# Kernel optimization log

Measured on AMD Instinct MI355X. Metric: run time of the kernel, lower is better.

Reference implementation:

```python
import jax, jax.numpy as jnp
import numpy as np

# Irreps config: input/output = 32x0e + 16x1o (dim 80), H=4 heads -> head = 8x0e + 4x1o (dim 20)
M0, M1 = 32, 16      # input muls for 0e / 1o
m0, m1 = 8, 4        # per-head muls
H = 4
HEAD_DIM = m0 + 3 * m1   # 20
WNUM = H * (M0 * m0 + M1 * m0 + M0 * m1 + M1 * m1)  # 2304 per-edge TP weights
NB, HID = 16, 64
SQRT3 = np.float32(np.sqrt(3.0))
EPS = 1e-8


def radial_mlp(x, W1, b1, W2, b2):
    return jax.nn.silu(x @ W1 + b1) @ W2 + b2


def tp_edge(ss, vv, sh0, sh1, w):
    """FullyConnectedTensorProduct (32x0e+16x1o) x (1x0e+1x1o) -> H*(8x0e+4x1o) with per-edge weights w [E, WNUM].
    Paths: 0e*0e->0e, 1o*1o->0e (CG dot/sqrt3), 0e*1o->1o, 1o*0e->1o; path norm 1/sqrt(fan_in)."""
    E = ss.shape[0]
    per = M0 * m0 + M1 * m0 + M0 * m1 + M1 * m1  # 576
    w = w.reshape(E, H, per)
    o = 0
    Wss = w[..., o:o + M0 * m0].reshape(E, H, M0, m0); o += M0 * m0
    Wvv = w[..., o:o + M1 * m0].reshape(E, H, M1, m0); o += M1 * m0
    Wsv = w[..., o:o + M0 * m1].reshape(E, H, M0, m1); o += M0 * m1
    Wvs = w[..., o:o + M1 * m1].reshape(E, H, M1, m1)
    fan = np.float32(np.sqrt(M0 + M1))  # fan_in = 48 for both output irreps
    vv_dot = jnp.einsum('eui,ei->eu', vv, sh1) / SQRT3
    out0 = (jnp.einsum('eu,ehuw->ehw', ss * sh0[:, None], Wss)
            + jnp.einsum('eu,ehuw->ehw', vv_dot, Wvv)) / fan          # [E,H,m0]
    out1 = (jnp.einsum('eu,ehuw->ehw', ss, Wsv)[..., None] * sh1[:, None, None, :]
            + jnp.einsum('eui,ehuw->ehwi', vv * sh0[:, None, None], Wvs)) / fan  # [E,H,m1,3]
    return out0, out1


def setup_inputs() -> dict:
    key = jax.random.key(0)
    ks = jax.random.split(key, 24)
    N, E = 2000, 32000
    g = lambda k, s, sc=1.0: jax.random.normal(k, s, jnp.float32) * sc
    inp = {}
    inp['node_features'] = g(ks[0], (N, M0 + 3 * M1))
    inp['edge_index'] = jax.random.randint(ks[1], (2, E), 0, N)
    inp['edge_sh'] = g(ks[2], (E, 4))
    inp['edge_radial_emb'] = jax.random.uniform(ks[3], (E, NB), jnp.float32)
    # query e3nn Linear (per-head blocks)
    inp['Wq0'] = g(ks[4], (H, M0, m0))
    inp['Wq1'] = g(ks[5], (H, M1, m1))
    # radial MLPs for key / value TP weights
    inp['Wk1'] = g(ks[6], (NB, HID), 1 / np.sqrt(NB)); inp['bk1'] = jnp.zeros((HID,), jnp.float32)
    inp['Wk2'] = g(ks[7], (HID, WNUM), 1 / np.sqrt(HID)); inp['bk2'] = jnp.zeros((WNUM,), jnp.float32)
    inp['Wv1'] = g(ks[8], (NB, HID), 1 / np.sqrt(NB)); inp['bv1'] = jnp.zeros((HID,), jnp.float32)
    inp['Wv2'] = g(ks[9], (HID, WNUM), 1 / np.sqrt(HID)); inp['bv2'] = jnp.zeros((WNUM,), jnp.float32)
    # single-head dot-product TP -> 0e (shared weights)
    inp['Wd0'] = g(ks[10], (m0, m0))
    inp['Wd1'] = g(ks[11], (m1, m1))
    # output projection Linear (all heads mixed per irrep)
    inp['Wo0'] = g(ks[12], (H * m0, M0))
    inp['Wo1'] = g(ks[13], (H * m1, M1))
    # FFN: out irreps -> (2*M0)x0e + M1x1o -> out irreps
    inp['Wf1_0'] = g(ks[14], (M0, 2 * M0))
    inp['Wf1_1'] = g(ks[15], (M1, M1))
    inp['Wf2_0'] = g(ks[16], (2 * M0, M0))
    inp['Wf2_1'] = g(ks[17], (M1, M1))
    return inp


def reference(node_features, edge_index, edge_sh, edge_radial_emb,
              Wq0, Wq1, Wk1, bk1, Wk2, bk2, Wv1, bv1, Wv2, bv2,
              Wd0, Wd1, Wo0, Wo1, Wf1_0, Wf1_1, Wf2_0, Wf2_1):
    N = node_features.shape[0]
    s = node_features[:, :M0]                       # [N, M0] scalars
    v = node_features[:, M0:].reshape(N, M1, 3)     # [N, M1, 3] vectors
    src, dst = edge_index[0], edge_index[1]

    # query Linear (e3nn: per-irrep channel mix, norm 1/sqrt(fan_in))
    q0 = jnp.einsum('nu,huw->nhw', s, Wq0) / np.sqrt(M0)
    q1 = jnp.einsum('nui,huw->nhwi', v, Wq1) / np.sqrt(M1)

    sh0, sh1 = edge_sh[:, 0], edge_sh[:, 1:4]
    ss, vv = s[src], v[src]                         # gather per edge

    wk = radial_mlp(edge_radial_emb, Wk1, bk1, Wk2, bk2)
    wv = radial_mlp(edge_radial_emb, Wv1, bv1, Wv2, bv2)
    k0, k1 = tp_edge(ss, vv, sh0, sh1, wk)
    v0, v1 = tp_edge(ss, vv, sh0, sh1, wv)

    # per-head equivariant dot product -> 0e logits
    qd0, qd1 = q0[dst], q1[dst]
    fan_d = np.float32(np.sqrt(m0 * m0 + m1 * m1))
    logits = (jnp.einsum('ehu,uv,ehv->eh', qd0, Wd0, k0)
              + jnp.einsum('ehui,uv,ehvi->eh', qd1, Wd1, k1) / SQRT3) / fan_d
    logits = logits / np.sqrt(HEAD_DIM)             # self.scale
    logits = jnp.clip(logits, -10.0, 10.0)

    # scatter softmax over edges sharing a destination node
    seg_max = jax.ops.segment_max(logits, dst, num_segments=N)
    seg_max = jnp.maximum(seg_max, -10.0)           # handle empty segments
    ex = jnp.exp(logits - seg_max[dst])
    denom = jax.ops.segment_sum(ex, dst, num_segments=N)
    alpha = ex / (denom[dst] + 1e-12)               # [E, H]

    agg0 = jax.ops.segment_sum(alpha[..., None] * v0, dst, num_segments=N)        # [N,H,m0]
    agg1 = jax.ops.segment_sum(alpha[..., None, None] * v1, dst, num_segments=N)  # [N,H,m1,3]

    # output projection Linear over concatenated heads
    o0 = agg0.reshape(N, H * m0) @ Wo0 / np.sqrt(H * m0)
    o1 = jnp.einsum('nui,uw->nwi', agg1.reshape(N, H * m1, 3), Wo1) / np.sqrt(H * m1)

    # residual (input irreps == output irreps -> identity skip)
    x0 = s + o0
    x1 = v + o1

    # FFN with SafeNormActivation
    f0 = x0 @ Wf1_0 / np.sqrt(M0)                               # [N, 2*M0]
    f1 = jnp.einsum('nui,uw->nwi', x1, Wf1_1) / np.sqrt(M1)     # [N, M1, 3]
    a0 = jax.nn.silu(f0)
    norms = jnp.linalg.norm(f1, axis=-1, keepdims=True)
    safe = jnp.maximum(norms, EPS)
    a1 = jnp.where(norms < EPS, 0.0, (f1 / safe) * jax.nn.silu(norms))
    g0 = a0 @ Wf2_0 / np.sqrt(2 * M0)
    g1 = jnp.einsum('nui,uw->nwi', a1, Wf2_1) / np.sqrt(M1)

    out0 = x0 + g0
    out1 = x1 + g1
    return jnp.concatenate([out0, out1.reshape(N, M1 * 3)], axis=-1)
```

## Files before the change

kernel.cpp:

```cpp
#include <hip/hip_runtime.h>

typedef unsigned int uint;
typedef unsigned short ushort;
typedef __attribute__((ext_vector_type(8))) short bf16x8;
typedef __attribute__((ext_vector_type(4))) float f32x4;
typedef __attribute__((ext_vector_type(2))) float f32x2;

#define N_NODES 2000
#define N_EDGES 32000
#define WNUM 2304

constexpr size_t OFF_AGG0 = 0;
constexpr size_t OFF_AGG1 = 64000;
constexpr size_t OFF_DEN  = 160000;
constexpr size_t OFF_FLAG = 170000;
constexpr size_t OFF_W2T  = 170004;
constexpr size_t OFF_QT0  = 317460;
constexpr size_t OFF_QT1  = 381460;
constexpr size_t OFF_W1T  = 509460;
constexpr size_t OFF_W1P  = 511508;

__device__ __forceinline__ float b2f(ushort u){ union{uint i; float f;}x; x.i=((uint)u)<<16; return x.f; }
__device__ __forceinline__ float lo16(uint w){ union{uint u; float f;}x; x.u=w<<16; return x.f; }
__device__ __forceinline__ float hi16(uint w){ union{uint u; float f;}x; x.u=w&0xFFFF0000u; return x.f; }
__device__ __forceinline__ ushort f2b(float f){
  union{float f; uint u;}x; x.f=f;
  uint r = (x.u + 0x7FFFu + ((x.u>>16)&1u)) >> 16;
  return (ushort)r;
}
__device__ __forceinline__ float siluf(float x){ return x / (1.f + __expf(-x)); }

template<bool F32>
__device__ __forceinline__ float ldf(const void* p, int i){
  if (F32) return ((const float*)p)[i];
  return b2f(((const ushort*)p)[i]);
}
__device__ __forceinline__ float ldfr(const void* p, int i, bool f32){
  return f32 ? ((const float*)p)[i] : b2f(((const ushort*)p)[i]);
}

template<bool F32>
__device__ void prep_body(
    const void* __restrict__ nf,
    const void* __restrict__ Wk2, const void* __restrict__ Wv2,
    const void* __restrict__ Wk1, const void* __restrict__ Wv1,
    const void* __restrict__ Wq0, const void* __restrict__ Wq1,
    const void* __restrict__ Wd0, const void* __restrict__ Wd1,
    ushort* __restrict__ W2T, float* __restrict__ W1T, uint* __restrict__ W1P,
    float* __restrict__ qt0, float* __restrict__ qt1){
  const int t = threadIdx.x;
  const int bid = blockIdx.x;

  if (bid < 72){
    __shared__ ushort tile[64][66];
    const int mat = bid / 36, jt = bid - mat*36;
    const void* W = mat ? Wv2 : Wk2;
    const int j0 = jt*64;
    const int jo = t & 63, cb = t >> 6;
    #pragma unroll
    for (int k=0; k<16; ++k){
      const int c = cb + k*4;
      tile[c][jo] = F32 ? f2b(((const float*)W)[(size_t)c*WNUM + j0 + jo])
                        : ((const ushort*)W)[(size_t)c*WNUM + j0 + jo];
    }
    __syncthreads();
    const int jl = t >> 2, c0 = (t & 3)*16;
    ushort* dst = W2T + (size_t)mat*147456 + (size_t)(j0+jl)*64 + c0;
    #pragma unroll
    for (int k=0; k<16; ++k) dst[k] = tile[c0+k][jl];
  } else if (bid < 104){
    __shared__ float nfL[64][80];
    __shared__ float wq0L[1024], wq1L[256], wd0L[64], wd1L[16];
    const int nb = bid - 72, n0 = nb*64;
    for (int idx=t; idx<64*80; idx+=256){
      const int nn = n0 + idx/80;
      nfL[idx/80][idx%80] = (nn < N_NODES) ? ldf<F32>(nf, nn*80 + idx%80) : 0.f;
    }
    for (int idx=t; idx<1024; idx+=256) wq0L[idx] = ldf<F32>(Wq0, idx);
    if (t < 256) wq1L[t] = ldf<F32>(Wq1, t);
    if (t < 64)  wd0L[t] = ldf<F32>(Wd0, t);
    if (t < 16)  wd1L[t] = ldf<F32>(Wd1, t);
    __syncthreads();
    const int nl = t >> 2, h = t & 3;
    const int nn = n0 + nl;
    if (nn < N_NODES){
      const float* S = &nfL[nl][0];
      float q0[8];
      #pragma unroll
      for (int w=0; w<8; ++w){
        float a = 0.f;
        #pragma unroll
        for (int u=0; u<32; ++u) a += S[u]*wq0L[h*256 + u*8 + w];
        q0[w] = a * 0.17677669529663687f;
      }
      #pragma unroll
      for (int vv=0; vv<8; ++vv){
        float a = 0.f;
        #pragma unroll
        for (int u=0; u<8; ++u) a += q0[u]*wd0L[u*8+vv];
        qt0[nn*32 + h*8 + vv] = a;
      }
      float q1[12];
      #pragma unroll
      for (int w=0; w<4; ++w)
        #pragma unroll
        for (int i=0; i<3; ++i){
          float a = 0.f;
          #pragma unroll
          for (int u=0; u<16; ++u) a += S[32+u*3+i]*wq1L[h*64 + u*4 + w];
          q1[w*3+i] = a * 0.25f;
        }
      #pragma unroll
      for (int vv=0; vv<4; ++vv)
        #pragma unroll
        for (int i=0; i<3; ++i){
          float a = 0.f;
          #pragma unroll
          for (int u=0; u<4; ++u) a += q1[u*3+i]*wd1L[u*4+vv];
          qt1[nn*48 + h*12 + vv*3 + i] = a;
        }
    }
  } else {
    for (int idx=t; idx<2048; idx+=256){
      const int mat = idx >> 10, rem = idx & 1023;
      const int c = rem >> 4, b = rem & 15;
      W1T[idx] = ldf<F32>(mat ? Wv1 : Wk1, b*64 + c);
    }
    for (int idx=t; idx<1024; idx+=256){
      const int mat = idx >> 9, rem = idx & 511;
      const int c = rem >> 3, j = rem & 7;
      const void* W = mat ? Wv1 : Wk1;
      ushort u0, u1;
      if (F32){ u0 = f2b(((const float*)W)[(2*j)*64+c]); u1 = f2b(((const float*)W)[(2*j+1)*64+c]); }
      else    { u0 = ((const ushort*)W)[(2*j)*64+c];     u1 = ((const ushort*)W)[(2*j+1)*64+c]; }
      W1P[idx] = (uint)u0 | ((uint)u1 << 16);
    }
  }
}

__global__ __launch_bounds__(256) void prep_kernel(
    const void* nf,
    const void* Wk2, const void* Wv2,
    const void* Wk1, const void* Wv1,
    const void* Wq0, const void* Wq1,
    const void* Wd0, const void* Wd1,
    ushort* W2T, float* W1T, uint* W1P, float* qt0, float* qt1,
    int* flag){
  __shared__ int s_cnt;
  const int t = threadIdx.x;
  if (t == 0) s_cnt = 0;
  __syncthreads();
  {
    uint u = ((const ushort*)nf)[t*2];
    uint ex = (u >> 7) & 0xFFu;
    if (ex >= 0xA0u) atomicAdd(&s_cnt, 1);
  }
  __syncthreads();
  const bool F32 = (s_cnt >= 20);
  if (blockIdx.x == 0 && t == 0) *flag = F32 ? 1 : 0;
  if (F32) prep_body<true >(nf, Wk2, Wv2, Wk1, Wv1, Wq0, Wq1, Wd0, Wd1, W2T, W1T, W1P, qt0, qt1);
  else     prep_body<false>(nf, Wk2, Wv2, Wk1, Wv1, Wq0, Wq1, Wd0, Wd1, W2T, W1T, W1P, qt0, qt1);
}

struct Smem {
  ushort hidA[4096];
  union {
    struct {
      float fssT[32][34];
      float fvvT[16][34];
      float sslT[32][34];
    } f;
    float cont[2688];
  } u;
  float vshT[3][16][34];
  float sh1T[3][34];
  int   dstL[32];
};

__device__ __forceinline__ f32x4 mma_pair(const bf16x8& a0f, const bf16x8& a1f,
                                          bf16x8 b0, bf16x8 b1, float bb){
  f32x4 c = {bb,bb,bb,bb};
  c = __builtin_amdgcn_mfma_f32_16x16x32_bf16(a0f, b0, c, 0,0,0);
  c = __builtin_amdgcn_mfma_f32_16x16x32_bf16(a1f, b1, c, 0,0,0);
  return c;
}
__device__ __forceinline__ void acc_feat(const f32x4 c, const float* fp, float* acc){
  f32x2 fA = *(const f32x2*)(fp);
  f32x2 fB = *(const f32x2*)(fp + 2);
  acc[0] += c[0]*fA[0]; acc[1] += c[1]*fA[1];
  acc[2] += c[2]*fB[0]; acc[3] += c[3]*fB[1];
}

template<bool F32>
__device__ void edge_body(
    const void* __restrict__ nf,  const int* __restrict__ eidx,
    const void* __restrict__ esh, const void* __restrict__ emb,
    const float* __restrict__ W1T, const uint* __restrict__ W1P,
    const void* __restrict__ bk1, const void* __restrict__ bk2,
    const void* __restrict__ bv1, const void* __restrict__ bv2,
    const ushort* __restrict__ W2T,
    const float* __restrict__ qt0g, const float* __restrict__ qt1g,
    float* __restrict__ agg0, float* __restrict__ agg1, float* __restrict__ denom,
    Smem& sm){
  const int t  = threadIdx.x;
  const int hw = t >> 5;
  const int r  = t & 31;
  const int geb = blockIdx.x*32;

  int geA[4], srcA[4], dstA[4];
  float shv0[4], shv1[4], shv2[4], shv3[4];
  #pragma unroll
  for (int e=0; e<4; ++e) geA[e] = geb + hw*4 + e;
  #pragma unroll
  for (int e=0; e<4; ++e){ srcA[e] = eidx[geA[e]]; dstA[e] = eidx[N_EDGES + geA[e]]; }
  #pragma unroll
  for (int e=0; e<4; ++e){
    if (F32){
      float4 s4 = ((const float4*)esh)[geA[e]];
      shv0[e]=s4.x; shv1[e]=s4.y; shv2[e]=s4.z; shv3[e]=s4.w;
    } else {
      uint2 u2 = ((const uint2*)esh)[geA[e]];
      shv0[e]=lo16(u2.x); shv1[e]=hi16(u2.x); shv2[e]=lo16(u2.y); shv3[e]=hi16(u2.y);
    }
  }
  #pragma unroll
  for (int e=0; e<4; ++e){
    const int le = hw*4+e, src = srcA[e];
    const float sh0 = shv0[e], s1a = shv1[e], s1b = shv2[e], s1c = shv3[e];
    if (r == 0) sm.dstL[le] = dstA[e];
    if (r < 3) sm.sh1T[r][le] = (r==0)? s1a : (r==1)? s1b : s1c;
    float sv = ldf<F32>(nf, src*80 + r);
    sm.u.f.sslT[r][le] = sv;
    sm.u.f.fssT[r][le] = sv * sh0;
    if (r < 16){
      float v0 = ldf<F32>(nf, src*80+32+r*3+0);
      float v1 = ldf<F32>(nf, src*80+32+r*3+1);
      float v2 = ldf<F32>(nf, src*80+32+r*3+2);
      sm.vshT[0][r][le] = v0*sh0; sm.vshT[1][r][le] = v1*sh0; sm.vshT[2][r][le] = v2*sh0;
      sm.u.f.fvvT[r][le] = (v0*s1a + v1*s1b + v2*s1c) * 0.5773502691896258f;
    }
  }

  {
    float bkv[2], bvv[2];
    f32x4 wkF[2][4], wvF[2][4];
    uint4 wkB[2][2], wvB[2][2];
    #pragma unroll
    for (int cc=0; cc<2; ++cc){
      const int c = r + cc*32;
      bkv[cc] = ldf<F32>(bk1, c); bvv[cc] = ldf<F32>(bv1, c);
      if (F32){
        const f32x4* pk = (const f32x4*)(W1T + c*16);
        const f32x4* pv = (const f32x4*)(W1T + 1024 + c*16);
        wkF[cc][0]=pk[0]; wkF[cc][1]=pk[1]; wkF[cc][2]=pk[2]; wkF[cc][3]=pk[3];
        wvF[cc][0]=pv[0]; wvF[cc][1]=pv[1]; wvF[cc][2]=pv[2]; wvF[cc][3]=pv[3];
      } else {
        const uint4* pk = (const uint4*)(W1P + c*8);
        const uint4* pv = (const uint4*)(W1P + 512 + c*8);
        wkB[cc][0]=pk[0]; wkB[cc][1]=pk[1];
        wvB[cc][0]=pv[0]; wvB[cc][1]=pv[1];
      }
    }
    uint4 ra, rb; float4 fa, fb, fc, fd;
    if (F32){
      const float4* p = (const float4*)emb + (size_t)geA[0]*4;
      fa = p[0]; fb = p[1]; fc = p[2]; fd = p[3];
    } else {
      const uint4* p = (const uint4*)emb + (size_t)geA[0]*2;
      ra = p[0]; rb = p[1];
    }
    #pragma unroll
    for (int e=0; e<4; ++e){
      float em[16];
      if (F32){
        em[0]=fa.x; em[1]=fa.y; em[2]=fa.z; em[3]=fa.w;
        em[4]=fb.x; em[5]=fb.y; em[6]=fb.z; em[7]=fb.w;
        em[8]=fc.x; em[9]=fc.y; em[10]=fc.z; em[11]=fc.w;
        em[12]=fd.x; em[13]=fd.y; em[14]=fd.z; em[15]=fd.w;
      } else {
        em[0]=lo16(ra.x); em[1]=hi16(ra.x); em[2]=lo16(ra.y); em[3]=hi16(ra.y);
        em[4]=lo16(ra.z); em[5]=hi16(ra.z); em[6]=lo16(ra.w); em[7]=hi16(ra.w);
        em[8]=lo16(rb.x); em[9]=hi16(rb.x); em[10]=lo16(rb.y); em[11]=hi16(rb.y);
        em[12]=lo16(rb.z); em[13]=hi16(rb.z); em[14]=lo16(rb.w); em[15]=hi16(rb.w);
      }
      if (e < 3){
        if (F32){
          const float4* p = (const float4*)emb + (size_t)geA[e+1]*4;
          fa = p[0]; fb = p[1]; fc = p[2]; fd = p[3];
        } else {
          const uint4* p = (const uint4*)emb + (size_t)geA[e+1]*2;
          ra = p[0]; rb = p[1];
        }
      }
      const int le = hw*4+e;
      #pragma unroll
      for (int cc=0; cc<2; ++cc){
        const int c = r + cc*32;
        float ak = bkv[cc], av = bvv[cc];
        if (F32){
          #pragma unroll
          for (int g=0; g<4; ++g)
            #pragma unroll
            for (int j=0; j<4; ++j){
              ak += em[g*4+j]*wkF[cc][g][j];
              av += em[g*4+j]*wvF[cc][g][j];
            }
        } else {
          #pragma unroll
          for (int g=0; g<2; ++g){
            const uint4 a = wkB[cc][g], b = wvB[cc][g];
            ak += em[g*8+0]*lo16(a.x) + em[g*8+1]*hi16(a.x)
                + em[g*8+2]*lo16(a.y) + em[g*8+3]*hi16(a.y)
                + em[g*8+4]*lo16(a.z) + em[g*8+5]*hi16(a.z)
                + em[g*8+6]*lo16(a.w) + em[g*8+7]*hi16(a.w);
            av += em[g*8+0]*lo16(b.x) + em[g*8+1]*hi16(b.x)
                + em[g*8+2]*lo16(b.y) + em[g*8+3]*hi16(b.y)
                + em[g*8+4]*lo16(b.z) + em[g*8+5]*hi16(b.z)
                + em[g*8+6]*lo16(b.w) + em[g*8+7]*hi16(b.w);
          }
        }
        const int idx = (le>>4)*1024 + (c>>5)*512 + ((((c>>3)&3)*16 + (le&15))<<3) + (c&7);
        sm.hidA[idx]        = f2b(siluf(ak));
        sm.hidA[2048 + idx] = f2b(siluf(av));
      }
    }
  }
  __syncthreads();

  const int h = t >> 6;
  const int lane = t & 63, q = lane >> 4, n = lane & 15;
  const float invfan = 0.14433756729740643f;
  float exv[2][4];

  const ushort* wbase = W2T + h*36864 + n*64 + q*8;
  const int bi0 = h*576 + n;
  const float* fb_ss = &sm.u.f.fssT[n>>3][q*4];
  const float* fb_sl = &sm.u.f.sslT[n>>2][q*4];
  const int nq2 = n>>2;

  #pragma unroll 1
  for (int kv=0; kv<2; ++kv){
    const ushort* wptr = wbase + kv*147456;
    const void* bvec = kv ? bv2 : bk2;
    bf16x8 af[2][2];
    #pragma unroll
    for (int Mt=0; Mt<2; ++Mt)
      #pragma unroll
      for (int kh=0; kh<2; ++kh)
        af[Mt][kh] = *(const bf16x8*)&sm.hidA[kv*2048 + Mt*1024 + kh*512 + lane*8];

    float a0[2][4], aP[2][4], aW[3][2][4];
    #pragma unroll
    for (int Mt=0; Mt<2; ++Mt)
      #pragma unroll
      for (int z=0; z<4; ++z){
        a0[Mt][z]=0.f; aP[Mt][z]=0.f;
        aW[0][Mt][z]=0.f; aW[1][Mt][z]=0.f; aW[2][Mt][z]=0.f;
      }

#define PREF(P0,P1,PB,TL) \
  P0 = *(const bf16x8*)(wptr + (TL)*1024); \
  P1 = *(const bf16x8*)(wptr + (TL)*1024 + 32); \
  PB = ldf<F32>(bvec, bi0 + (TL)*16);

    bf16x8 pA0, pA1, pB0, pB1; float pAb, pBb;
    PREF(pA0, pA1, pAb, 0);
    PREF(pB0, pB1, pBb, 1);

    #pragma unroll 2
    for (int tl=0; tl<24; tl+=2){
      { bf16x8 b0=pA0, b1=pA1; float bb=pAb;
        PREF(pA0, pA1, pAb, tl+2);
        const float* fp = fb_ss + tl*68;
        #pragma unroll
        for (int Mt=0; Mt<2; ++Mt) acc_feat(mma_pair(af[Mt][0], af[Mt][1], b0, b1, bb), fp + Mt*16, a0[Mt]); }
      { bf16x8 b0=pB0, b1=pB1; float bb=pBb;
        PREF(pB0, pB1, pBb, tl+3);
        const float* fp = fb_ss + (tl+1)*68;
        #pragma unroll
        for (int Mt=0; Mt<2; ++Mt) acc_feat(mma_pair(af[Mt][0], af[Mt][1], b0, b1, bb), fp + Mt*16, a0[Mt]); }
    }
    #pragma unroll 2
    for (int tl=24; tl<32; tl+=2){
      { bf16x8 b0=pA0, b1=pA1; float bb=pAb;
        PREF(pA0, pA1, pAb, tl+2);
        const float* fp = fb_sl + (tl-24)*136;
        #pragma unroll
        for (int Mt=0; Mt<2; ++Mt) acc_feat(mma_pair(af[Mt][0], af[Mt][1], b0, b1, bb), fp + Mt*16, aP[Mt]); }
      { bf16x8 b0=pB0, b1=pB1; float bb=pBb;
        PREF(pB0, pB1, pBb, tl+3);
        const float* fp = fb_sl + (tl-23)*136;
        #pragma unroll
        for (int Mt=0; Mt<2; ++Mt) acc_feat(mma_pair(af[Mt][0], af[Mt][1], b0, b1, bb), fp + Mt*16, aP[Mt]); }
    }
#define BODY_AW(B0,B1,BB,TL) { \
    const int u = ((TL)-32)*4 + nq2; \
    _Pragma("unroll") \
    for (int Mt=0; Mt<2; ++Mt){ \
      f32x4 c = mma_pair(af[Mt][0], af[Mt][1], B0, B1, BB); \
      _Pragma("unroll") \
      for (int i=0; i<3; ++i) acc_feat(c, &sm.vshT[i][u][Mt*16+q*4], aW[i][Mt]); \
    } }
    { bf16x8 b0=pA0, b1=pA1; float bb=pAb; PREF(pA0, pA1, pAb, 34); BODY_AW(b0,b1,bb,32); }
    { bf16x8 b0=pB0, b1=pB1; float bb=pBb; PREF(pB0, pB1, pBb, 35); BODY_AW(b0,b1,bb,33); }
    { bf16x8 b0=pA0, b1=pA1; float bb=pAb; BODY_AW(b0,b1,bb,34); }
    { bf16x8 b0=pB0, b1=pB1; float bb=pBb; BODY_AW(b0,b1,bb,35); }
#undef BODY_AW
#undef PREF

    #pragma unroll
    for (int Mt=0; Mt<2; ++Mt)
      #pragma unroll
      for (int z=0; z<4; ++z){
        a0[Mt][z] += __shfl_xor(a0[Mt][z], 8, 64);
        aP[Mt][z] += __shfl_xor(aP[Mt][z], 4, 64);
        aP[Mt][z] += __shfl_xor(aP[Mt][z], 8, 64);
        #pragma unroll
        for (int i=0; i<3; ++i){
          aW[i][Mt][z] += __shfl_xor(aW[i][Mt][z], 4, 64);
          aW[i][Mt][z] += __shfl_xor(aW[i][Mt][z], 8, 64);
        }
      }

    if (kv == 0){
      float lgp[2][4];
      #pragma unroll
      for (int Mt=0; Mt<2; ++Mt)
        #pragma unroll
        for (int z=0; z<4; ++z){
          const int el = Mt*16 + q*4 + z;
          const int d = sm.dstL[el];
          float acc = 0.f;
          if (n < 8) acc = qt0g[d*32 + h*8 + n] * a0[Mt][z];
          if (n < 4){
            float s = 0.f;
            #pragma unroll
            for (int i=0; i<3; ++i){
              float k1 = aP[Mt][z]*sm.sh1T[i][el] + aW[i][Mt][z];
              s += qt1g[d*48 + h*12 + n*3 + i] * k1;
            }
            acc += s * 0.5773502691896258f;
          }
          lgp[Mt][z] = acc;
        }
      #pragma unroll
      for (int Mt=0; Mt<2; ++Mt)
        #pragma unroll
        for (int z=0; z<4; ++z){
          lgp[Mt][z] += __shfl_xor(lgp[Mt][z], 1, 64);
          lgp[Mt][z] += __shfl_xor(lgp[Mt][z], 2, 64);
          lgp[Mt][z] += __shfl_xor(lgp[Mt][z], 4, 64);
          lgp[Mt][z] += __shfl_xor(lgp[Mt][z], 8, 64);
          float lg = lgp[Mt][z] * invfan * 0.025f;
          lg = fminf(10.f, fmaxf(-10.f, lg));
          exv[Mt][z] = __expf(lg - 10.0f);
        }
    } else {
      __syncthreads();
      #pragma unroll
      for (int Mt=0; Mt<2; ++Mt)
        #pragma unroll
        for (int z=0; z<4; ++z){
          const int el = Mt*16 + q*4 + z;
          const float ex = exv[Mt][z];
          float* cp = &sm.u.cont[el*84 + h*21];
          if (n == 0) cp[0] = ex;
          if (n < 8)  cp[1+n] = ex * a0[Mt][z] * invfan;
          if (n < 4){
            #pragma unroll
            for (int i=0; i<3; ++i){
              float v1 = (aP[Mt][z]*sm.sh1T[i][el] + aW[i][Mt][z]) * invfan;
              cp[9+n*3+i] = ex * v1;
            }
          }
        }
    }
  }
  __syncthreads();

  #pragma unroll
  for (int k=0; k<11; ++k){
    const int idx = t + k*256;
    if (idx < 2688){
      const int el = idx / 84;
      const int cm = idx - el*84;
      const int h2 = cm / 21;
      const int comp = cm - h2*21;
      const float val = sm.u.cont[idx];
      const int d2 = sm.dstL[el];
      if (comp == 0)      atomicAdd(denom + d2*4  + h2, val);
      else if (comp < 9)  atomicAdd(agg0  + d2*32 + h2*8  + (comp-1), val);
      else                atomicAdd(agg1  + d2*48 + h2*12 + (comp-9), val);
    }
  }
}

__global__ __launch_bounds__(256) void edge_kernel(
    const void* nf, const int* eidx, const void* esh, const void* emb,
    const float* W1T, const uint* W1P,
    const void* bk1, const void* bk2,
    const void* bv1, const void* bv2,
    const ushort* W2T, const float* qt0g, const float* qt1g,
    float* agg0, float* agg1, float* denom, const int* flag){
  __shared__ Smem sm;
  if (*flag)
    edge_body<true >(nf,eidx,esh,emb,W1T,W1P,bk1,bk2,bv1,bv2,W2T,qt0g,qt1g,agg0,agg1,denom,sm);
  else
    edge_body<false>(nf,eidx,esh,emb,W1T,W1P,bk1,bk2,bv1,bv2,W2T,qt0g,qt1g,agg0,agg1,denom,sm);
}

__global__ __launch_bounds__(256) void node_out_kernel(
    const void* __restrict__ nf, const float* __restrict__ agg0r, const float* __restrict__ agg1r,
    const float* __restrict__ denom,
    const void* __restrict__ Wo0, const void* __restrict__ Wo1,
    const void* __restrict__ Wf10, const void* __restrict__ Wf11,
    const void* __restrict__ Wf20, const void* __restrict__ Wf21,
    void* __restrict__ out, const int* __restrict__ flag){
  __shared__ float ag0[4][32], ag1[4][48], adiv[4][4];
  __shared__ float x0s[4][32], x1s[4][48], a0s[4][64], f1s[4][48], coefs[4][16];
  const bool F32 = (*flag) != 0;
  const int s = threadIdx.x >> 6, t = threadIdx.x & 63;
  const int n = blockIdx.x*4 + s;
  if (t < 4) adiv[s][t] = 1.f / (denom[n*4+t] + 1e-12f);
  __syncthreads();
  if (t < 32) ag0[s][t] = agg0r[n*32+t] * adiv[s][t>>3];
  if (t < 48) ag1[s][t] = agg1r[n*48+t] * adiv[s][t/12];
  __syncthreads();
  if (t < 32){
    float o = 0.f;
    #pragma unroll
    for (int k=0; k<32; ++k) o += ag0[s][k]*ldfr(Wo0, k*32+t, F32);
    x0s[s][t] = ldfr(nf, n*80+t, F32) + o*0.17677669529663687f;
  }
  if (t < 48){
    int w = t/3, i = t - w*3;
    float o = 0.f;
    #pragma unroll
    for (int u=0; u<16; ++u) o += ag1[s][u*3+i]*ldfr(Wo1, u*16+w, F32);
    x1s[s][t] = ldfr(nf, n*80+32+t, F32) + o*0.25f;
  }
  __syncthreads();
  {
    float f0 = 0.f;
    #pragma unroll
    for (int u=0; u<32; ++u) f0 += x0s[s][u]*ldfr(Wf10, u*64+t, F32);
    a0s[s][t] = siluf(f0*0.17677669529663687f);
  }
  if (t < 48){
    int w = t/3, i = t - w*3;
    float f1 = 0.f;
    #pragma unroll
    for (int u=0; u<16; ++u) f1 += x1s[s][u*3+i]*ldfr(Wf11, u*16+w, F32);
    f1s[s][t] = f1*0.25f;
  }
  __syncthreads();
  if (t < 16){
    float a = f1s[s][t*3], b = f1s[s][t*3+1], c = f1s[s][t*3+2];
    float nrm = sqrtf(a*a+b*b+c*c);
    float safe = fmaxf(nrm, 1e-8f);
    coefs[s][t] = (nrm < 1e-8f) ? 0.f : siluf(nrm)/safe;
  }
  __syncthreads();
  if (t < 32){
    float g = 0.f;
    #pragma unroll
    for (int u=0; u<64; ++u) g += a0s[s][u]*ldfr(Wf20, u*32+t, F32);
    float val = x0s[s][t] + g*0.125f;
    if (F32) ((float*)out)[n*80+t] = val; else ((ushort*)out)[n*80+t] = f2b(val);
  }
  if (t < 48){
    int w = t/3, i = t - w*3;
    float g = 0.f;
    #pragma unroll
    for (int u=0; u<16; ++u) g += coefs[s][u]*f1s[s][u*3+i]*ldfr(Wf21, u*16+w, F32);
    float val = x1s[s][t] + g*0.25f;
    if (F32) ((float*)out)[n*80+32+t] = val; else ((ushort*)out)[n*80+32+t] = f2b(val);
  }
}

extern "C" void kernel_launch(void* const* d_in, const int* in_sizes, int n_in,
                              void* d_out, int out_size, void* d_ws, size_t ws_size,
                              hipStream_t stream){
  const void* nf   = d_in[0];
  const int*  eidx = (const int*)d_in[1];
  const void* esh  = d_in[2];
  const void* emb  = d_in[3];
  const void* Wq0  = d_in[4];
  const void* Wq1  = d_in[5];
  const void* Wk1  = d_in[6];
  const void* bk1  = d_in[7];
  const void* Wk2  = d_in[8];
  const void* bk2  = d_in[9];
  const void* Wv1  = d_in[10];
  const void* bv1  = d_in[11];
  const void* Wv2  = d_in[12];
  const void* bv2  = d_in[13];
  const void* Wd0  = d_in[14];
  const void* Wd1  = d_in[15];
  const void* Wo0  = d_in[16];
  const void* Wo1  = d_in[17];
  const void* Wf10 = d_in[18];
  const void* Wf11 = d_in[19];
  const void* Wf20 = d_in[20];
  const void* Wf21 = d_in[21];
  float* ws = (float*)d_ws;

  float* agg0  = ws + OFF_AGG0;
  float* agg1  = ws + OFF_AGG1;
  float* denom = ws + OFF_DEN;
  int*   flag  = (int*)(ws + OFF_FLAG);
  ushort* W2T  = (ushort*)(ws + OFF_W2T);
  float* qt0   = ws + OFF_QT0;
  float* qt1   = ws + OFF_QT1;
  float* W1T   = ws + OFF_W1T;
  uint*  W1P   = (uint*)(ws + OFF_W1P);

  hipMemsetAsync(agg0, 0, 168000*sizeof(float), stream);
  prep_kernel<<<105, 256, 0, stream>>>(nf, Wk2, Wv2, Wk1, Wv1, Wq0, Wq1, Wd0, Wd1,
                                       W2T, W1T, W1P, qt0, qt1, flag);
  edge_kernel<<<N_EDGES/32, 256, 0, stream>>>(nf, eidx, esh, emb,
                                              W1T, W1P, bk1, bk2, bv1, bv2,
                                              W2T, qt0, qt1,
                                              agg0, agg1, denom, flag);
  node_out_kernel<<<N_NODES/4, 256, 0, stream>>>(nf, agg0, agg1, denom,
                                                 Wo0, Wo1, Wf10, Wf11, Wf20, Wf21, d_out, flag);
}
```

Measured before the change: 219.9 us.

## Process 64 edges per block with key/value waves running concurrently

The edge kernel now handles 64 edges per 512-thread block instead of 32 per 256 threads. Each wave owns one (key/value, head) pair, so the key and value MFMA passes run in parallel on separate waves rather than in a serial loop. Per-edge intermediates are parked in shared memory and the softmax exponentials pass through an LDS buffer. Each W2 B-fragment load now feeds four M-tiles instead of two, halving global weight traffic per edge, at the cost of more LDS, more registers and fewer blocks in flight.

```diff
diff --git a/kernel.cpp b/kernel.cpp
--- a/kernel.cpp
+++ b/kernel.cpp
@@ -163,18 +163,21 @@
 }
 
 struct Smem {
-  ushort hidA[4096];
+  ushort hidA[8192];
   union {
     struct {
-      float fssT[32][34];
-      float fvvT[16][34];
-      float sslT[32][34];
+      float fssT[32][66];
+      float fvvT[16][66];
+      float sslT[32][66];
     } f;
-    float cont[2688];
+    float cont[5376];
   } u;
-  float vshT[3][16][34];
-  float sh1T[3][34];
-  int   dstL[32];
+  float vshT[3][16][66];
+  float sh1T[3][66];
+  float park0[2][4][64][8];
+  float parkP[2][4][64][4];
+  float exL[64][4];
+  int   dstL[64];
 };
 
 __device__ __forceinline__ f32x4 mma_pair(const bf16x8& a0f, const bf16x8& a1f,
@@ -203,74 +206,73 @@
     float* __restrict__ agg0, float* __restrict__ agg1, float* __restrict__ denom,
     Smem& sm){
   const int t  = threadIdx.x;
-  const int hw = t >> 5;
-  const int r  = t & 31;
-  const int geb = blockIdx.x*32;
-
-  int geA[4], srcA[4], dstA[4];
-  float shv0[4], shv1[4], shv2[4], shv3[4];
-  #pragma unroll
-  for (int e=0; e<4; ++e) geA[e] = geb + hw*4 + e;
-  #pragma unroll
-  for (int e=0; e<4; ++e){ srcA[e] = eidx[geA[e]]; dstA[e] = eidx[N_EDGES + geA[e]]; }
-  #pragma unroll
-  for (int e=0; e<4; ++e){
+  const int geb = blockIdx.x*64;
+
+  {
+    const int g = t >> 5, r = t & 31;
+    int geA[4], srcA[4], dstA[4];
+    float shv0[4], shv1[4], shv2[4], shv3[4];
+    #pragma unroll
+    for (int e=0; e<4; ++e) geA[e] = geb + g*4 + e;
+    #pragma unroll
+    for (int e=0; e<4; ++e){ srcA[e] = eidx[geA[e]]; dstA[e] = eidx[N_EDGES + geA[e]]; }
+    #pragma unroll
+    for (int e=0; e<4; ++e){
+      if (F32){
+        float4 s4 = ((const float4*)esh)[geA[e]];
+        shv0[e]=s4.x; shv1[e]=s4.y; shv2[e]=s4.z; shv3[e]=s4.w;
+      } else {
+        uint2 u2 = ((const uint2*)esh)[geA[e]];
+        shv0[e]=lo16(u2.x); shv1[e]=hi16(u2.x); shv2[e]=lo16(u2.y); shv3[e]=hi16(u2.y);
+      }
+    }
+    #pragma unroll
+    for (int e=0; e<4; ++e){
+      const int le = g*4+e, src = srcA[e];
+      const float sh0 = shv0[e], s1a = shv1[e], s1b = shv2[e], s1c = shv3[e];
+      if (r == 0) sm.dstL[le] = dstA[e];
+      if (r < 3) sm.sh1T[r][le] = (r==0)? s1a : (r==1)? s1b : s1c;
+      float sv = ldf<F32>(nf, src*80 + r);
+      sm.u.f.sslT[r][le] = sv;
+      sm.u.f.fssT[r][le] = sv * sh0;
+      if (r < 16){
+        float v0 = ldf<F32>(nf, src*80+32+r*3+0);
+        float v1 = ldf<F32>(nf, src*80+32+r*3+1);
+        float v2 = ldf<F32>(nf, src*80+32+r*3+2);
+        sm.vshT[0][r][le] = v0*sh0; sm.vshT[1][r][le] = v1*sh0; sm.vshT[2][r][le] = v2*sh0;
+        sm.u.f.fvvT[r][le] = (v0*s1a + v1*s1b + v2*s1c) * 0.5773502691896258f;
+      }
+    }
+  }
+
+  {
+    const int c  = t & 63;
+    const int g8 = t >> 6;
+    const int le0 = g8*8;
+    float bkv = ldf<F32>(bk1, c), bvv = ldf<F32>(bv1, c);
+    f32x4 wkF[4], wvF[4];
+    uint4 wkB[2], wvB[2];
     if (F32){
-      float4 s4 = ((const float4*)esh)[geA[e]];
-      shv0[e]=s4.x; shv1[e]=s4.y; shv2[e]=s4.z; shv3[e]=s4.w;
+      const f32x4* pk = (const f32x4*)(W1T + c*16);
+      const f32x4* pv = (const f32x4*)(W1T + 1024 + c*16);
+      wkF[0]=pk[0]; wkF[1]=pk[1]; wkF[2]=pk[2]; wkF[3]=pk[3];
+      wvF[0]=pv[0]; wvF[1]=pv[1]; wvF[2]=pv[2]; wvF[3]=pv[3];
     } else {
-      uint2 u2 = ((const uint2*)esh)[geA[e]];
-      shv0[e]=lo16(u2.x); shv1[e]=hi16(u2.x); shv2[e]=lo16(u2.y); shv3[e]=hi16(u2.y);
-    }
-  }
-  #pragma unroll
-  for (int e=0; e<4; ++e){
-    const int le = hw*4+e, src = srcA[e];
-    const float sh0 = shv0[e], s1a = shv1[e], s1b = shv2[e], s1c = shv3[e];
-    if (r == 0) sm.dstL[le] = dstA[e];
-    if (r < 3) sm.sh1T[r][le] = (r==0)? s1a : (r==1)? s1b : s1c;
-    float sv = ldf<F32>(nf, src*80 + r);
-    sm.u.f.sslT[r][le] = sv;
-    sm.u.f.fssT[r][le] = sv * sh0;
-    if (r < 16){
-      float v0 = ldf<F32>(nf, src*80+32+r*3+0);
-      float v1 = ldf<F32>(nf, src*80+32+r*3+1);
-      float v2 = ldf<F32>(nf, src*80+32+r*3+2);
-      sm.vshT[0][r][le] = v0*sh0; sm.vshT[1][r][le] = v1*sh0; sm.vshT[2][r][le] = v2*sh0;
-      sm.u.f.fvvT[r][le] = (v0*s1a + v1*s1b + v2*s1c) * 0.5773502691896258f;
-    }
-  }
-
-  {
-    float bkv[2], bvv[2];
-    f32x4 wkF[2][4], wvF[2][4];
-    uint4 wkB[2][2], wvB[2][2];
-    #pragma unroll
-    for (int cc=0; cc<2; ++cc){
-      const int c = r + cc*32;
-      bkv[cc] = ldf<F32>(bk1, c); bvv[cc] = ldf<F32>(bv1, c);
-      if (F32){
-        const f32x4* pk = (const f32x4*)(W1T + c*16);
-        const f32x4* pv = (const f32x4*)(W1T + 1024 + c*16);
-        wkF[cc][0]=pk[0]; wkF[cc][1]=pk[1]; wkF[cc][2]=pk[2]; wkF[cc][3]=pk[3];
-        wvF[cc][0]=pv[0]; wvF[cc][1]=pv[1]; wvF[cc][2]=pv[2]; wvF[cc][3]=pv[3];
-      } else {
-        const uint4* pk = (const uint4*)(W1P + c*8);
-        const uint4* pv = (const uint4*)(W1P + 512 + c*8);
-        wkB[cc][0]=pk[0]; wkB[cc][1]=pk[1];
-        wvB[cc][0]=pv[0]; wvB[cc][1]=pv[1];
-      }
+      const uint4* pk = (const uint4*)(W1P + c*8);
+      const uint4* pv = (const uint4*)(W1P + 512 + c*8);
+      wkB[0]=pk[0]; wkB[1]=pk[1];
+      wvB[0]=pv[0]; wvB[1]=pv[1];
     }
     uint4 ra, rb; float4 fa, fb, fc, fd;
     if (F32){
-      const float4* p = (const float4*)emb + (size_t)geA[0]*4;
+      const float4* p = (const float4*)emb + (size_t)(geb+le0)*4;
       fa = p[0]; fb = p[1]; fc = p[2]; fd = p[3];
     } else {
-      const uint4* p = (const uint4*)emb + (size_t)geA[0]*2;
+      const uint4* p = (const uint4*)emb + (size_t)(geb+le0)*2;
       ra = p[0]; rb = p[1];
     }
     #pragma unroll
-    for (int e=0; e<4; ++e){
+    for (int e=0; e<8; ++e){
       float em[16];
       if (F32){
         em[0]=fa.x; em[1]=fa.y; em[2]=fa.z; em[3]=fa.w;
@@ -283,205 +285,227 @@
         em[8]=lo16(rb.x); em[9]=hi16(rb.x); em[10]=lo16(rb.y); em[11]=hi16(rb.y);
         em[12]=lo16(rb.z); em[13]=hi16(rb.z); em[14]=lo16(rb.w); em[15]=hi16(rb.w);
       }
-      if (e < 3){
+      if (e < 7){
         if (F32){
-          const float4* p = (const float4*)emb + (size_t)geA[e+1]*4;
+          const float4* p = (const float4*)emb + (size_t)(geb+le0+e+1)*4;
           fa = p[0]; fb = p[1]; fc = p[2]; fd = p[3];
         } else {
-          const uint4* p = (const uint4*)emb + (size_t)geA[e+1]*2;
+          const uint4* p = (const uint4*)emb + (size_t)(geb+le0+e+1)*2;
           ra = p[0]; rb = p[1];
         }
       }
-      const int le = hw*4+e;
-      #pragma unroll
-      for (int cc=0; cc<2; ++cc){
-        const int c = r + cc*32;
-        float ak = bkv[cc], av = bvv[cc];
-        if (F32){
+      const int le = le0+e;
+      float ak = bkv, av = bvv;
+      if (F32){
+        #pragma unroll
+        for (int g=0; g<4; ++g)
           #pragma unroll
-          for (int g=0; g<4; ++g)
-            #pragma unroll
-            for (int j=0; j<4; ++j){
-              ak += em[g*4+j]*wkF[cc][g][j];
-              av += em[g*4+j]*wvF[cc][g][j];
-            }
-        } else {
-          #pragma unroll
-          for (int g=0; g<2; ++g){
-            const uint4 a = wkB[cc][g], b = wvB[cc][g];
-            ak += em[g*8+0]*lo16(a.x) + em[g*8+1]*hi16(a.x)
-                + em[g*8+2]*lo16(a.y) + em[g*8+3]*hi16(a.y)
-                + em[g*8+4]*lo16(a.z) + em[g*8+5]*hi16(a.z)
-                + em[g*8+6]*lo16(a.w) + em[g*8+7]*hi16(a.w);
-            av += em[g*8+0]*lo16(b.x) + em[g*8+1]*hi16(b.x)
-                + em[g*8+2]*lo16(b.y) + em[g*8+3]*hi16(b.y)
-                + em[g*8+4]*lo16(b.z) + em[g*8+5]*hi16(b.z)
-                + em[g*8+6]*lo16(b.w) + em[g*8+7]*hi16(b.w);
+          for (int j=0; j<4; ++j){
+            ak += em[g*4+j]*wkF[g][j];
+            av += em[g*4+j]*wvF[g][j];
           }
+      } else {
+        #pragma unroll
+        for (int g=0; g<2; ++g){
+          const uint4 a = wkB[g], b = wvB[g];
+          ak += em[g*8+0]*lo16(a.x) + em[g*8+1]*hi16(a.x)
+              + em[g*8+2]*lo16(a.y) + em[g*8+3]*hi16(a.y)
+              + em[g*8+4]*lo16(a.z) + em[g*8+5]*hi16(a.z)
+              + em[g*8+6]*lo16(a.w) + em[g*8+7]*hi16(a.w);
+          av += em[g*8+0]*lo16(b.x) + em[g*8+1]*hi16(b.x)
+              + em[g*8+2]*lo16(b.y) + em[g*8+3]*hi16(b.y)
+              + em[g*8+4]*lo16(b.z) + em[g*8+5]*hi16(b.z)
+              + em[g*8+6]*lo16(b.w) + em[g*8+7]*hi16(b.w);
         }
-        const int idx = (le>>4)*1024 + (c>>5)*512 + ((((c>>3)&3)*16 + (le&15))<<3) + (c&7);
-        sm.hidA[idx]        = f2b(siluf(ak));
-        sm.hidA[2048 + idx] = f2b(siluf(av));
-      }
-    }
-  }
-  __syncthreads();
-
-  const int h = t >> 6;
+      }
+      const int idx = (le>>4)*1024 + (c>>5)*512 + ((((c>>3)&3)*16 + (le&15))<<3) + (c&7);
+      sm.hidA[idx]        = f2b(siluf(ak));
+      sm.hidA[4096 + idx] = f2b(siluf(av));
+    }
+  }
+  __syncthreads();
+
+  const int w  = t >> 6;
+  const int kv = w >> 2;
+  const int h  = w & 3;
   const int lane = t & 63, q = lane >> 4, n = lane & 15;
   const float invfan = 0.14433756729740643f;
-  float exv[2][4];
-
-  const ushort* wbase = W2T + h*36864 + n*64 + q*8;
+
+  const ushort* wptr = W2T + (size_t)kv*147456 + h*36864 + n*64 + q*8;
+  const void* bvec = kv ? bv2 : bk2;
   const int bi0 = h*576 + n;
   const float* fb_ss = &sm.u.f.fssT[n>>3][q*4];
   const float* fb_sl = &sm.u.f.sslT[n>>2][q*4];
   const int nq2 = n>>2;
 
-  #pragma unroll 1
-  for (int kv=0; kv<2; ++kv){
-    const ushort* wptr = wbase + kv*147456;
-    const void* bvec = kv ? bv2 : bk2;
-    bf16x8 af[2][2];
-    #pragma unroll
-    for (int Mt=0; Mt<2; ++Mt)
-      #pragma unroll
-      for (int kh=0; kh<2; ++kh)
-        af[Mt][kh] = *(const bf16x8*)&sm.hidA[kv*2048 + Mt*1024 + kh*512 + lane*8];
-
-    float a0[2][4], aP[2][4], aW[3][2][4];
-    #pragma unroll
-    for (int Mt=0; Mt<2; ++Mt)
-      #pragma unroll
-      for (int z=0; z<4; ++z){
-        a0[Mt][z]=0.f; aP[Mt][z]=0.f;
-        aW[0][Mt][z]=0.f; aW[1][Mt][z]=0.f; aW[2][Mt][z]=0.f;
-      }
+  bf16x8 af[4][2];
+  #pragma unroll
+  for (int Mt=0; Mt<4; ++Mt)
+    #pragma unroll
+    for (int kh=0; kh<2; ++kh)
+      af[Mt][kh] = *(const bf16x8*)&sm.hidA[kv*4096 + Mt*1024 + kh*512 + lane*8];
 
 #define PREF(P0,P1,PB,TL) \
   P0 = *(const bf16x8*)(wptr + (TL)*1024); \
   P1 = *(const bf16x8*)(wptr + (TL)*1024 + 32); \
   PB = ldf<F32>(bvec, bi0 + (TL)*16);
 
-    bf16x8 pA0, pA1, pB0, pB1; float pAb, pBb;
-    PREF(pA0, pA1, pAb, 0);
-    PREF(pB0, pB1, pBb, 1);
-
+  bf16x8 pA0, pA1, pB0, pB1; float pAb, pBb;
+  PREF(pA0, pA1, pAb, 0);
+  PREF(pB0, pB1, pBb, 1);
+
+  {
+    float a0[4][4];
+    #pragma unroll
+    for (int Mt=0; Mt<4; ++Mt){ a0[Mt][0]=0.f; a0[Mt][1]=0.f; a0[Mt][2]=0.f; a0[Mt][3]=0.f; }
     #pragma unroll 2
     for (int tl=0; tl<24; tl+=2){
       { bf16x8 b0=pA0, b1=pA1; float bb=pAb;
         PREF(pA0, pA1, pAb, tl+2);
-        const float* fp = fb_ss + tl*68;
-        #pragma unroll
-        for (int Mt=0; Mt<2; ++Mt) acc_feat(mma_pair(af[Mt][0], af[Mt][1], b0, b1, bb), fp + Mt*16, a0[Mt]); }
+        const float* fp = fb_ss + tl*132;
+        #pragma unroll
+        for (int Mt=0; Mt<4; ++Mt) acc_feat(mma_pair(af[Mt][0], af[Mt][1], b0, b1, bb), fp + Mt*16, a0[Mt]); }
       { bf16x8 b0=pB0, b1=pB1; float bb=pBb;
         PREF(pB0, pB1, pBb, tl+3);
-        const float* fp = fb_ss + (tl+1)*68;
-        #pragma unroll
-        for (int Mt=0; Mt<2; ++Mt) acc_feat(mma_pair(af[Mt][0], af[Mt][1], b0, b1, bb), fp + Mt*16, a0[Mt]); }
-    }
+        const float* fp = fb_ss + (tl+1)*132;
+        #pragma unroll
+        for (int Mt=0; Mt<4; ++Mt) acc_feat(mma_pair(af[Mt][0], af[Mt][1], b0, b1, bb), fp + Mt*16, a0[Mt]); }
+    }
+    #pragma unroll
+    for (int Mt=0; Mt<4; ++Mt)
+      #pragma unroll
+      for (int z=0; z<4; ++z){
+        a0[Mt][z] += __shfl_xor(a0[Mt][z], 8, 64);
+        if (n < 8) sm.park0[kv][h][Mt*16 + q*4 + z][n] = a0[Mt][z];
+      }
+  }
+
+  {
+    float aP[4][4];
+    #pragma unroll
+    for (int Mt=0; Mt<4; ++Mt){ aP[Mt][0]=0.f; aP[Mt][1]=0.f; aP[Mt][2]=0.f; aP[Mt][3]=0.f; }
     #pragma unroll 2
     for (int tl=24; tl<32; tl+=2){
       { bf16x8 b0=pA0, b1=pA1; float bb=pAb;
         PREF(pA0, pA1, pAb, tl+2);
-        const float* fp = fb_sl + (tl-24)*136;
-        #pragma unroll
-        for (int Mt=0; Mt<2; ++Mt) acc_feat(mma_pair(af[Mt][0], af[Mt][1], b0, b1, bb), fp + Mt*16, aP[Mt]); }
+        const float* fp = fb_sl + (tl-24)*264;
+        #pragma unroll
+        for (int Mt=0; Mt<4; ++Mt) acc_feat(mma_pair(af[Mt][0], af[Mt][1], b0, b1, bb), fp + Mt*16, aP[Mt]); }
       { bf16x8 b0=pB0, b1=pB1; float bb=pBb;
         PREF(pB0, pB1, pBb, tl+3);
-        const float* fp = fb_sl + (tl-23)*136;
-        #pragma unroll
-        for (int Mt=0; Mt<2; ++Mt) acc_feat(mma_pair(af[Mt][0], af[Mt][1], b0, b1, bb), fp + Mt*16, aP[Mt]); }
-    }
+        const float* fp = fb_sl + (tl-23)*264;
+        #pragma unroll
+        for (int Mt=0; Mt<4; ++Mt) acc_feat(mma_pair(af[Mt][0], af[Mt][1], b0, b1, bb), fp + Mt*16, aP[Mt]); }
+    }
+    #pragma unroll
+    for (int Mt=0; Mt<4; ++Mt)
+      #pragma unroll
+      for (int z=0; z<4; ++z){
+        aP[Mt][z] += __shfl_xor(aP[Mt][z], 4, 64);
+        aP[Mt][z] += __shfl_xor(aP[Mt][z], 8, 64);
+        if (n < 4) sm.parkP[kv][h][Mt*16 + q*4 + z][n] = aP[Mt][z];
+      }
+  }
+
+  float aW[3][4][4];
+  #pragma unroll
+  for (int i=0; i<3; ++i)
+    #pragma unroll
+    for (int Mt=0; Mt<4; ++Mt){ aW[i][Mt][0]=0.f; aW[i][Mt][1]=0.f; aW[i][Mt][2]=0.f; aW[i][Mt][3]=0.f; }
 #define BODY_AW(B0,B1,BB,TL) { \
     const int u = ((TL)-32)*4 + nq2; \
     _Pragma("unroll") \
-    for (int Mt=0; Mt<2; ++Mt){ \
+    for (int Mt=0; Mt<4; ++Mt){ \
       f32x4 c = mma_pair(af[Mt][0], af[Mt][1], B0, B1, BB); \
       _Pragma("unroll") \
       for (int i=0; i<3; ++i) acc_feat(c, &sm.vshT[i][u][Mt*16+q*4], aW[i][Mt]); \
     } }
-    { bf16x8 b0=pA0, b1=pA1; float bb=pAb; PREF(pA0, pA1, pAb, 34); BODY_AW(b0,b1,bb,32); }
-    { bf16x8 b0=pB0, b1=pB1; float bb=pBb; PREF(pB0, pB1, pBb, 35); BODY_AW(b0,b1,bb,33); }
-    { bf16x8 b0=pA0, b1=pA1; float bb=pAb; BODY_AW(b0,b1,bb,34); }
-    { bf16x8 b0=pB0, b1=pB1; float bb=pBb; BODY_AW(b0,b1,bb,35); }
+  { bf16x8 b0=pA0, b1=pA1; float bb=pAb; PREF(pA0, pA1, pAb, 34); BODY_AW(b0,b1,bb,32); }
+  { bf16x8 b0=pB0, b1=pB1; float bb=pBb; PREF(pB0, pB1, pBb, 35); BODY_AW(b0,b1,bb,33); }
+  { bf16x8 b0=pA0, b1=pA1; float bb=pAb; BODY_AW(b0,b1,bb,34); }
+  { bf16x8 b0=pB0, b1=pB1; float bb=pBb; BODY_AW(b0,b1,bb,35); }
 #undef BODY_AW
 #undef PREF
-
-    #pragma unroll
-    for (int Mt=0; Mt<2; ++Mt)
+  #pragma unroll
+  for (int i=0; i<3; ++i)
+    #pragma unroll
+    for (int Mt=0; Mt<4; ++Mt)
       #pragma unroll
       for (int z=0; z<4; ++z){
-        a0[Mt][z] += __shfl_xor(a0[Mt][z], 8, 64);
-        aP[Mt][z] += __shfl_xor(aP[Mt][z], 4, 64);
-        aP[Mt][z] += __shfl_xor(aP[Mt][z], 8, 64);
-        #pragma unroll
-        for (int i=0; i<3; ++i){
-          aW[i][Mt][z] += __shfl_xor(aW[i][Mt][z], 4, 64);
-          aW[i][Mt][z] += __shfl_xor(aW[i][Mt][z], 8, 64);
+        aW[i][Mt][z] += __shfl_xor(aW[i][Mt][z], 4, 64);
+        aW[i][Mt][z] += __shfl_xor(aW[i][Mt][z], 8, 64);
+      }
+
+  if (kv == 0){
+    float lgp[4][4];
+    #pragma unroll
+    for (int Mt=0; Mt<4; ++Mt)
+      #pragma unroll
+      for (int z=0; z<4; ++z){
+        const int el = Mt*16 + q*4 + z;
+        const int d = sm.dstL[el];
+        float acc = 0.f;
+        if (n < 8) acc = qt0g[d*32 + h*8 + n] * sm.park0[0][h][el][n];
+        if (n < 4){
+          const float aPv = sm.parkP[0][h][el][n];
+          float s = 0.f;
+          #pragma unroll
+          for (int i=0; i<3; ++i){
+            float k1 = aPv*sm.sh1T[i][el] + aW[i][Mt][z];
+            s += qt1g[d*48 + h*12 + n*3 + i] * k1;
+          }
+          acc += s * 0.5773502691896258f;
         }
-      }
-
-    if (kv == 0){
-      float lgp[2][4];
-      #pragma unroll
-      for (int Mt=0; Mt<2; ++Mt)
+        lgp[Mt][z] = acc;
+      }
+    #pragma unroll
+    for (int Mt=0; Mt<4; ++Mt)
+      #pragma unroll
+      for (int z=0; z<4; ++z){
+        lgp[Mt][z] += __shfl_xor(lgp[Mt][z], 1, 64);
+        lgp[Mt][z] += __shfl_xor(lgp[Mt][z], 2, 64);
+        lgp[Mt][z] += __shfl_xor(lgp[Mt][z], 4, 64);
+        lgp[Mt][z] += __shfl_xor(lgp[Mt][z], 8, 64);
+      }
+    if (n == 0){
+      #pragma unroll
+      for (int Mt=0; Mt<4; ++Mt)
         #pragma unroll
         for (int z=0; z<4; ++z){
-          const int el = Mt*16 + q*4 + z;
-          const int d = sm.dstL[el];
-          float acc = 0.f;
-          if (n < 8) acc = qt0g[d*32 + h*8 + n] * a0[Mt][z];
-          if (n < 4){
-            float s = 0.f;
-            #pragma unroll
-            for (int i=0; i<3; ++i){
-              float k1 = aP[Mt][z]*sm.sh1T[i][el] + aW[i][Mt][z];
-              s += qt1g[d*48 + h*12 + n*3 + i] * k1;
-            }
-            acc += s * 0.5773502691896258f;
-          }
-          lgp[Mt][z] = acc;
-        }
-      #pragma unroll
-      for (int Mt=0; Mt<2; ++Mt)
-        #pragma unroll
-        for (int z=0; z<4; ++z){
-          lgp[Mt][z] += __shfl_xor(lgp[Mt][z], 1, 64);
-          lgp[Mt][z] += __shfl_xor(lgp[Mt][z], 2, 64);
-          lgp[Mt][z] += __shfl_xor(lgp[Mt][z], 4, 64);
-          lgp[Mt][z] += __shfl_xor(lgp[Mt][z], 8, 64);
           float lg = lgp[Mt][z] * invfan * 0.025f;
           lg = fminf(10.f, fmaxf(-10.f, lg));
-          exv[Mt][z] = __expf(lg - 10.0f);
+          sm.exL[Mt*16 + q*4 + z][h] = __expf(lg - 10.0f);
         }
-    } else {
-      __syncthreads();
-      #pragma unroll
-      for (int Mt=0; Mt<2; ++Mt)
-        #pragma unroll
-        for (int z=0; z<4; ++z){
-          const int el = Mt*16 + q*4 + z;
-          const float ex = exv[Mt][z];
-          float* cp = &sm.u.cont[el*84 + h*21];
-          if (n == 0) cp[0] = ex;
-          if (n < 8)  cp[1+n] = ex * a0[Mt][z] * invfan;
-          if (n < 4){
-            #pragma unroll
-            for (int i=0; i<3; ++i){
-              float v1 = (aP[Mt][z]*sm.sh1T[i][el] + aW[i][Mt][z]) * invfan;
-              cp[9+n*3+i] = ex * v1;
-            }
+    }
+  }
+  __syncthreads();
+
+  if (kv == 1){
+    #pragma unroll
+    for (int Mt=0; Mt<4; ++Mt)
+      #pragma unroll
+      for (int z=0; z<4; ++z){
+        const int el = Mt*16 + q*4 + z;
+        const float ex = sm.exL[el][h];
+        float* cp = &sm.u.cont[el*84 + h*21];
+        if (n == 0) cp[0] = ex;
+        if (n < 8)  cp[1+n] = ex * sm.park0[1][h][el][n] * invfan;
+        if (n < 4){
+          const float aPv = sm.parkP[1][h][el][n];
+          #pragma unroll
+          for (int i=0; i<3; ++i){
+            float v1 = (aPv*sm.sh1T[i][el] + aW[i][Mt][z]) * invfan;
+            cp[9+n*3+i] = ex * v1;
           }
         }
-    }
+      }
   }
   __syncthreads();
 
   #pragma unroll
   for (int k=0; k<11; ++k){
-    const int idx = t + k*256;
-    if (idx < 2688){
+    const int idx = t + k*512;
+    if (idx < 5376){
       const int el = idx / 84;
       const int cm = idx - el*84;
       const int h2 = cm / 21;
@@ -495,7 +519,7 @@
   }
 }
 
-__global__ __launch_bounds__(256) void edge_kernel(
+__global__ __launch_bounds__(512, 4) void edge_kernel(
     const void* nf, const int* eidx, const void* esh, const void* emb,
     const float* W1T, const uint* W1P,
     const void* bk1, const void* bk2,
@@ -618,7 +642,7 @@
   hipMemsetAsync(agg0, 0, 168000*sizeof(float), stream);
   prep_kernel<<<105, 256, 0, stream>>>(nf, Wk2, Wv2, Wk1, Wv1, Wq0, Wq1, Wd0, Wd1,
                                        W2T, W1T, W1P, qt0, qt1, flag);
-  edge_kernel<<<N_EDGES/32, 256, 0, stream>>>(nf, eidx, esh, emb,
+  edge_kernel<<<N_EDGES/64, 512, 0, stream>>>(nf, eidx, esh, emb,
                                               W1T, W1P, bk1, bk2, bv1, bv2,
                                               W2T, qt0, qt1,
                                               agg0, agg1, denom, flag);
```

After: 229.2 us. 1.04x slower.
